# Kernel tuning notes

Hardware: AMD Instinct MI355X
Metric: run time of the kernel (lower is better)

## Reference

```python
import jax, jax.numpy as jnp
import numpy as np

LN_EPS = 1e-5
MODEL_DIM = 256
HEADS = 4


def layer_norm(x, gamma, beta):
    mu = jnp.mean(x, axis=-1, keepdims=True)
    var = jnp.var(x, axis=-1, keepdims=True)
    return (x - mu) * jax.lax.rsqrt(var + LN_EPS) * gamma + beta


def setup_inputs() -> dict:
    key = jax.random.key(0)
    ks = jax.random.split(key, 4)
    bs, s, d, h = 4, 2048, MODEL_DIM, HEADS
    x = jax.random.normal(ks[0], (bs, s, d), dtype=jnp.float32)
    Wq = jax.random.normal(ks[1], (d, h * d), dtype=jnp.float32) / np.sqrt(d)
    Wk = jax.random.normal(ks[2], (d, h * d), dtype=jnp.float32) / np.sqrt(d)
    Wv = jax.random.normal(ks[3], (h * d, d), dtype=jnp.float32) / np.sqrt(h * d)
    gamma = jnp.ones((d,), dtype=jnp.float32)
    beta = jnp.zeros((d,), dtype=jnp.float32)
    return {"x": x, "Wq": Wq, "Wk": Wk, "Wv": Wv, "gamma": gamma, "beta": beta}


def reference(x, Wq, Wk, Wv, gamma, beta):
    bs, s, d = x.shape
    h = Wq.shape[1] // d
    sqrt_norm = jnp.float32(np.sqrt(d))
    # pre_norm = False -> no input LN
    # NOTE: torch does .view(bs, h, s, d) on the (bs, s, h*d) projection --
    # a raw C-order reinterpretation, reproduced here by jnp.reshape.
    Q = jnp.reshape(x @ Wq, (bs, h, s, d))
    K = jnp.reshape(x @ Wk, (bs, h, s, d))
    scores = jnp.einsum('bhid,bhjd->bhij', Q, K)
    probs = jax.nn.softmax(scores / sqrt_norm, axis=-1)  # (bs, h, s, s)
    # value is the shared raw input x broadcast across heads
    out = jnp.einsum('bhij,bjd->bhid', probs, x)
    out = jnp.transpose(out, (0, 2, 1, 3)).reshape(bs, s, h * d)
    out = out @ Wv + x
    out = layer_norm(out, gamma, beta)  # post-norm
    return out, probs
```

## Files before the change

### kernel.cpp

```cpp
#include <hip/hip_runtime.h>

typedef __bf16 bf16;
typedef __bf16 bf16x8 __attribute__((ext_vector_type(8)));
typedef float f32x4 __attribute__((ext_vector_type(4)));

#define BS 4
#define S 2048
#define D 256
#define H 4
#define HD 1024
#define NROW 8192

__device__ __forceinline__ void load_lds16(const bf16* g, bf16* l) {
    __builtin_amdgcn_global_load_lds(
        (const __attribute__((address_space(1))) void*)g,
        (__attribute__((address_space(3))) void*)l, 16, 0, 0);
}

__global__ void prep_x(const float* __restrict__ x, bf16* __restrict__ x_bf,
                       bf16* __restrict__ xT_bf) {
    int idx = blockIdx.x * 256 + threadIdx.x;
    float v = x[idx];
    x_bf[idx] = (bf16)v;
    int dd = idx & (D - 1);
    int t = idx >> 8;
    int j = t & (S - 1);
    int b = t >> 11;
    xT_bf[(size_t)b * D * S + (size_t)dd * S + j] = (bf16)v;
}

__global__ void prep_w(const float* __restrict__ Wq, const float* __restrict__ Wk,
                       const float* __restrict__ Wv, bf16* __restrict__ WqT,
                       bf16* __restrict__ WkT, bf16* __restrict__ WvT) {
    int idx = blockIdx.x * 256 + threadIdx.x;
    const float SCALE = 0.09016844005556021f;
    int seg = idx >> 18;
    int r = idx & 262143;
    if (seg == 0) {
        int k = r & 255, n = r >> 8;
        WqT[r] = (bf16)(Wq[k * HD + n] * SCALE);
    } else if (seg == 1) {
        int k = r & 255, n = r >> 8;
        WkT[r] = (bf16)(Wk[k * HD + n]);
    } else {
        int k = r & 1023, n = r >> 10;
        WvT[r] = (bf16)(Wv[k * D + n]);
    }
}

__global__ __launch_bounds__(256) void gemm_nt_bf16(
    const bf16* __restrict__ A, const bf16* __restrict__ B0,
    const bf16* __restrict__ B1, bf16* __restrict__ C0, bf16* __restrict__ C1,
    int N, int Kd) {
    const bf16* B = blockIdx.z ? B1 : B0;
    bf16* C = blockIdx.z ? C1 : C0;
    int n0 = blockIdx.x * 64;
    int m0 = blockIdx.y * 64;
    __shared__ __align__(16) bf16 As[64 * 40];
    __shared__ __align__(16) bf16 Bs[64 * 40];
    int t = threadIdx.x, w = t >> 6, l = t & 63;
    int lr = l & 15, lq = l >> 4;
    f32x4 acc[4] = {};
    for (int k0 = 0; k0 < Kd; k0 += 32) {
        int row = t >> 2, cb = (t & 3) * 8;
        bf16x8 va = *(const bf16x8*)&A[(size_t)(m0 + row) * Kd + k0 + cb];
        *(bf16x8*)&As[row * 40 + cb] = va;
        bf16x8 vb = *(const bf16x8*)&B[(size_t)(n0 + row) * Kd + k0 + cb];
        *(bf16x8*)&Bs[row * 40 + cb] = vb;
        __syncthreads();
        bf16x8 af = *(const bf16x8*)&As[(w * 16 + lr) * 40 + lq * 8];
#pragma unroll
        for (int nt = 0; nt < 4; nt++) {
            bf16x8 bfr = *(const bf16x8*)&Bs[(nt * 16 + lr) * 40 + lq * 8];
            acc[nt] = __builtin_amdgcn_mfma_f32_16x16x32_bf16(af, bfr, acc[nt], 0, 0, 0);
        }
        __syncthreads();
    }
#pragma unroll
    for (int nt = 0; nt < 4; nt++)
#pragma unroll
        for (int rr = 0; rr < 4; rr++) {
            int row = m0 + w * 16 + lq * 4 + rr;
            C[(size_t)row * N + n0 + nt * 16 + lr] = (bf16)acc[nt][rr];
        }
}

__device__ __forceinline__ void stage_k_tile(const bf16* __restrict__ K,
                                             bf16* kb, int j0, int w, int l) {
    int krow = (w << 3) + (l >> 5);
    int kc = l & 31;
#pragma unroll
    for (int n = 0; n < 4; n++) {
        int r = krow + (n << 1);
        int cg = kc ^ ((r & 3) | ((r & 1) << 2));
        load_lds16(&K[(size_t)(j0 + r) * D + cg * 8], &kb[((w << 3) + (n << 1)) * 256]);
    }
}

__device__ __forceinline__ void stage_x_tile(const bf16* __restrict__ xTb,
                                             bf16* xb, int j0, int w, int l) {
    int xrow = (w << 6) + (l >> 2);
    int xc = l & 3;
#pragma unroll
    for (int n = 0; n < 4; n++) {
        int dd = xrow + (n << 4);
        int cg = xc ^ (dd & 3);
        load_lds16(&xTb[(size_t)dd * S + j0 + cg * 8], &xb[((w << 6) + (n << 4)) * 32]);
    }
}

__global__ __launch_bounds__(256, 2) void attn_fused(
    const bf16* __restrict__ Qbf, const bf16* __restrict__ Kbf,
    const bf16* __restrict__ xT, float* __restrict__ probs,
    bf16* __restrict__ attn) {
    int nblk = blockIdx.x;
    int lb = (nblk & 7) * 64 + (nblk >> 3);
    int bh = lb >> 5, b = bh >> 2, h = bh & 3;
    int t = threadIdx.x, w = t >> 6, l = t & 63;
    int lr = l & 15, lq = l >> 4;
    int sw = (lr & 3) | ((lr & 1) << 2);
    const bf16* Q = Qbf + (size_t)bh * S * D;
    const bf16* K = Kbf + (size_t)bh * S * D;
    const bf16* xTb = xT + (size_t)b * D * S;
    int ibase = (lb & 31) * 64 + w * 16;

    __shared__ __align__(16) bf16 kbuf[2][32 * 256];
    __shared__ __align__(16) bf16 xbuf[2][256 * 32];
    __shared__ __align__(16) bf16 pl[4][16 * 40];

    bf16x8 qf[8];
#pragma unroll
    for (int kf = 0; kf < 8; kf++)
        qf[kf] = *(const bf16x8*)&Q[(size_t)(ibase + lr) * D + kf * 32 + lq * 8];

    float lsum[4] = {0.f, 0.f, 0.f, 0.f};
    stage_k_tile(K, kbuf[0], 0, w, l);
    for (int it = 0; it < 64; it++) {
        int cur = it & 1;
        if (it < 63) {
            stage_k_tile(K, kbuf[cur ^ 1], (it + 1) << 5, w, l);
            asm volatile("s_waitcnt vmcnt(4)" ::: "memory");
        } else {
            asm volatile("s_waitcnt vmcnt(0)" ::: "memory");
        }
        __builtin_amdgcn_s_barrier();
#pragma unroll
        for (int subj = 0; subj < 2; subj++) {
            f32x4 acc = {};
#pragma unroll
            for (int kf = 0; kf < 8; kf++) {
                bf16x8 kfr = *(const bf16x8*)
                    &kbuf[cur][(subj * 16 + lr) * 256 + (((kf * 4 + lq) ^ sw) * 8)];
                acc = __builtin_amdgcn_mfma_f32_16x16x32_bf16(qf[kf], kfr, acc, 0, 0, 0);
            }
#pragma unroll
            for (int r = 0; r < 4; r++) lsum[r] += exp2f(acc[r]);
        }
        __builtin_amdgcn_s_barrier();
    }
    float li[4];
#pragma unroll
    for (int r = 0; r < 4; r++) {
        float s = lsum[r];
        for (int off = 1; off < 16; off <<= 1) s += __shfl_xor(s, off);
        li[r] = 1.0f / s;
    }

    f32x4 oacc[16] = {};
    float* probb = probs + (size_t)bh * S * S;
    stage_k_tile(K, kbuf[0], 0, w, l);
    stage_x_tile(xTb, xbuf[0], 0, w, l);
    for (int it = 0; it < 64; it++) {
        int cur = it & 1;
        int j0 = it << 5;
        if (it < 63) {
            stage_k_tile(K, kbuf[cur ^ 1], j0 + 32, w, l);
            stage_x_tile(xTb, xbuf[cur ^ 1], j0 + 32, w, l);
            asm volatile("s_waitcnt vmcnt(8)" ::: "memory");
        } else {
            asm volatile("s_waitcnt vmcnt(0)" ::: "memory");
        }
        __builtin_amdgcn_s_barrier();
#pragma unroll
        for (int subj = 0; subj < 2; subj++) {
            f32x4 acc = {};
#pragma unroll
            for (int kf = 0; kf < 8; kf++) {
                bf16x8 kfr = *(const bf16x8*)
                    &kbuf[cur][(subj * 16 + lr) * 256 + (((kf * 4 + lq) ^ sw) * 8)];
                acc = __builtin_amdgcn_mfma_f32_16x16x32_bf16(qf[kf], kfr, acc, 0, 0, 0);
            }
#pragma unroll
            for (int r = 0; r < 4; r++) {
                float p = exp2f(acc[r]) * li[r];
                pl[w][(lq * 4 + r) * 40 + subj * 16 + lr] = (bf16)p;
            }
        }
        bf16x8 pf = *(const bf16x8*)&pl[w][lr * 40 + lq * 8];
        f32x4 p0, p1;
#pragma unroll
        for (int e = 0; e < 4; e++) { p0[e] = (float)pf[e]; p1[e] = (float)pf[e + 4]; }
        float* pp = &probb[(size_t)(ibase + lr) * S + j0 + lq * 8];
        *(f32x4*)pp = p0;
        *(f32x4*)(pp + 4) = p1;
#pragma unroll
        for (int dt = 0; dt < 16; dt++) {
            int dd = dt * 16 + lr;
            bf16x8 xf = *(const bf16x8*)&xbuf[cur][dd * 32 + ((lq ^ (lr & 3)) * 8)];
            oacc[dt] = __builtin_amdgcn_mfma_f32_16x16x32_bf16(pf, xf, oacc[dt], 0, 0, 0);
        }
        __builtin_amdgcn_s_barrier();
    }
#pragma unroll
    for (int dt = 0; dt < 16; dt++)
#pragma unroll
        for (int rr = 0; rr < 4; rr++) {
            int row = ibase + lq * 4 + rr;
            attn[((size_t)(b * S + row)) * HD + h * D + dt * 16 + lr] = (bf16)oacc[dt][rr];
        }
}

__global__ __launch_bounds__(256) void out_gemm_ln(
    const bf16* __restrict__ attn, const bf16* __restrict__ WvT,
    const float* __restrict__ x, const float* __restrict__ gamma,
    const float* __restrict__ beta, float* __restrict__ out) {
    int m0 = blockIdx.x * 16;
    int t = threadIdx.x, w = t >> 6, l = t & 63;
    int lr = l & 15, lq = l >> 4;
    int ncol0 = w * 64;
    f32x4 acc[4] = {};
    for (int k0 = 0; k0 < HD; k0 += 32) {
        bf16x8 af = *(const bf16x8*)&attn[(size_t)(m0 + lr) * HD + k0 + lq * 8];
#pragma unroll
        for (int dt = 0; dt < 4; dt++) {
            bf16x8 bfr =
                *(const bf16x8*)&WvT[(size_t)(ncol0 + dt * 16 + lr) * HD + k0 + lq * 8];
            acc[dt] = __builtin_amdgcn_mfma_f32_16x16x32_bf16(af, bfr, acc[dt], 0, 0, 0);
        }
    }
    float sum[4] = {0, 0, 0, 0}, sq[4] = {0, 0, 0, 0};
#pragma unroll
    for (int dt = 0; dt < 4; dt++)
#pragma unroll
        for (int rr = 0; rr < 4; rr++) {
            int row = m0 + lq * 4 + rr;
            float v = acc[dt][rr] + x[(size_t)row * D + ncol0 + dt * 16 + lr];
            acc[dt][rr] = v;
            sum[rr] += v;
            sq[rr] += v * v;
        }
#pragma unroll
    for (int rr = 0; rr < 4; rr++)
        for (int off = 1; off < 16; off <<= 1) {
            sum[rr] += __shfl_xor(sum[rr], off);
            sq[rr] += __shfl_xor(sq[rr], off);
        }
    __shared__ float part[4][16][2];
    if (lr == 0)
#pragma unroll
        for (int rr = 0; rr < 4; rr++) {
            part[w][lq * 4 + rr][0] = sum[rr];
            part[w][lq * 4 + rr][1] = sq[rr];
        }
    __syncthreads();
    float mu[4], rs[4];
#pragma unroll
    for (int rr = 0; rr < 4; rr++) {
        int rowi = lq * 4 + rr;
        float s = part[0][rowi][0] + part[1][rowi][0] + part[2][rowi][0] + part[3][rowi][0];
        float q = part[0][rowi][1] + part[1][rowi][1] + part[2][rowi][1] + part[3][rowi][1];
        mu[rr] = s * (1.0f / 256.0f);
        float var = q * (1.0f / 256.0f) - mu[rr] * mu[rr];
        rs[rr] = rsqrtf(var + 1e-5f);
    }
#pragma unroll
    for (int dt = 0; dt < 4; dt++) {
        int col = ncol0 + dt * 16 + lr;
        float g = gamma[col], be = beta[col];
#pragma unroll
        for (int rr = 0; rr < 4; rr++) {
            float v = (acc[dt][rr] - mu[rr]) * rs[rr] * g + be;
            out[(size_t)(m0 + lq * 4 + rr) * D + col] = v;
        }
    }
}

extern "C" void kernel_launch(void* const* d_in, const int* in_sizes, int n_in,
                              void* d_out, int out_size, void* d_ws, size_t ws_size,
                              hipStream_t stream) {
    const float* x = (const float*)d_in[0];
    const float* Wq = (const float*)d_in[1];
    const float* Wk = (const float*)d_in[2];
    const float* Wv = (const float*)d_in[3];
    const float* gamma = (const float*)d_in[4];
    const float* beta = (const float*)d_in[5];
    float* out = (float*)d_out;
    float* probs = out + (size_t)NROW * D;

    char* ws = (char*)d_ws;
    bf16* x_bf = (bf16*)ws;
    bf16* xT_bf = (bf16*)(ws + 4194304);
    bf16* WqT = (bf16*)(ws + 8388608);
    bf16* WkT = (bf16*)(ws + 8912896);
    bf16* WvT = (bf16*)(ws + 9437184);
    bf16* Qbf = (bf16*)(ws + 9961472);
    bf16* Kbf = (bf16*)(ws + 26738688);
    bf16* attn = (bf16*)(ws + 43515904);

    prep_x<<<8192, 256, 0, stream>>>(x, x_bf, xT_bf);
    prep_w<<<3072, 256, 0, stream>>>(Wq, Wk, Wv, WqT, WkT, WvT);
    gemm_nt_bf16<<<dim3(16, 128, 2), 256, 0, stream>>>(x_bf, WqT, WkT, Qbf, Kbf,
                                                       HD, D);
    attn_fused<<<dim3(512), 256, 0, stream>>>(Qbf, Kbf, xT_bf, probs, attn);
    out_gemm_ln<<<512, 256, 0, stream>>>(attn, WvT, x, gamma, beta, out);
}
```

Measured before the change: 499.2 us.

## Tile transposes through LDS, stage full-K GEMM tiles, and retune LDS swizzles

After: 490.4 us. Within noise of the previous version (-1.8%).

```diff
diff --git a/kernel.cpp b/kernel.cpp
--- a/kernel.cpp
+++ b/kernel.cpp
@@ -1,6 +1,7 @@
 #include <hip/hip_runtime.h>
 
 typedef __bf16 bf16;
+typedef __bf16 bf16x4 __attribute__((ext_vector_type(4)));
 typedef __bf16 bf16x8 __attribute__((ext_vector_type(8)));
 typedef float f32x4 __attribute__((ext_vector_type(4)));
 
@@ -17,34 +18,86 @@
         (__attribute__((address_space(3))) void*)l, 16, 0, 0);
 }
 
-__global__ void prep_x(const float* __restrict__ x, bf16* __restrict__ x_bf,
-                       bf16* __restrict__ xT_bf) {
-    int idx = blockIdx.x * 256 + threadIdx.x;
-    float v = x[idx];
-    x_bf[idx] = (bf16)v;
-    int dd = idx & (D - 1);
-    int t = idx >> 8;
-    int j = t & (S - 1);
-    int b = t >> 11;
-    xT_bf[(size_t)b * D * S + (size_t)dd * S + j] = (bf16)v;
-}
-
-__global__ void prep_w(const float* __restrict__ Wq, const float* __restrict__ Wk,
-                       const float* __restrict__ Wv, bf16* __restrict__ WqT,
-                       bf16* __restrict__ WkT, bf16* __restrict__ WvT) {
-    int idx = blockIdx.x * 256 + threadIdx.x;
+__global__ __launch_bounds__(256) void prep_x(const float* __restrict__ x,
+                                              bf16* __restrict__ x_bf,
+                                              bf16* __restrict__ xT_bf) {
+    __shared__ bf16 tile[64][68];
+    int j0 = blockIdx.x * 64, d0 = blockIdx.y * 64, b = blockIdx.z;
+    int t = threadIdx.x;
+    int rsub = t >> 4;
+    int c4 = (t & 15) * 4;
+#pragma unroll
+    for (int rr = 0; rr < 4; rr++) {
+        int j = rr * 16 + rsub;
+        float4 v = *(const float4*)&x[((size_t)(b * S + j0 + j)) * D + d0 + c4];
+        bf16 b0 = (bf16)v.x, b1 = (bf16)v.y, b2 = (bf16)v.z, b3 = (bf16)v.w;
+        tile[j][c4 + 0] = b0;
+        tile[j][c4 + 1] = b1;
+        tile[j][c4 + 2] = b2;
+        tile[j][c4 + 3] = b3;
+        bf16x4 o = {b0, b1, b2, b3};
+        *(bf16x4*)&x_bf[((size_t)(b * S + j0 + j)) * D + d0 + c4] = o;
+    }
+    __syncthreads();
+#pragma unroll
+    for (int rr = 0; rr < 4; rr++) {
+        int dd = rr * 16 + rsub;
+        bf16x4 o;
+        o[0] = tile[c4 + 0][dd];
+        o[1] = tile[c4 + 1][dd];
+        o[2] = tile[c4 + 2][dd];
+        o[3] = tile[c4 + 3][dd];
+        *(bf16x4*)&xT_bf[(size_t)b * D * S + (size_t)(d0 + dd) * S + j0 + c4] = o;
+    }
+}
+
+__device__ __forceinline__ void tile_tr64(const float* __restrict__ src,
+                                          bf16* __restrict__ dst, int ldsrc,
+                                          int lddst, int r0, int c0, float scale,
+                                          bf16 (&tile)[64][68], int t) {
+    int rsub = t >> 4, c4 = (t & 15) * 4;
+#pragma unroll
+    for (int rr = 0; rr < 4; rr++) {
+        int r = rr * 16 + rsub;
+        float4 v = *(const float4*)&src[(size_t)(r0 + r) * ldsrc + c0 + c4];
+        tile[r][c4 + 0] = (bf16)(v.x * scale);
+        tile[r][c4 + 1] = (bf16)(v.y * scale);
+        tile[r][c4 + 2] = (bf16)(v.z * scale);
+        tile[r][c4 + 3] = (bf16)(v.w * scale);
+    }
+    __syncthreads();
+#pragma unroll
+    for (int rr = 0; rr < 4; rr++) {
+        int c = rr * 16 + rsub;
+        bf16x4 o;
+        o[0] = tile[c4 + 0][c];
+        o[1] = tile[c4 + 1][c];
+        o[2] = tile[c4 + 2][c];
+        o[3] = tile[c4 + 3][c];
+        *(bf16x4*)&dst[(size_t)(c0 + c) * lddst + r0 + c4] = o;
+    }
+}
+
+__global__ __launch_bounds__(256) void prep_w(const float* __restrict__ Wq,
+                                              const float* __restrict__ Wk,
+                                              const float* __restrict__ Wv,
+                                              bf16* __restrict__ WqT,
+                                              bf16* __restrict__ WkT,
+                                              bf16* __restrict__ WvT) {
+    __shared__ bf16 tile[64][68];
     const float SCALE = 0.09016844005556021f;
-    int seg = idx >> 18;
-    int r = idx & 262143;
-    if (seg == 0) {
-        int k = r & 255, n = r >> 8;
-        WqT[r] = (bf16)(Wq[k * HD + n] * SCALE);
-    } else if (seg == 1) {
-        int k = r & 255, n = r >> 8;
-        WkT[r] = (bf16)(Wk[k * HD + n]);
+    int bx = blockIdx.x, t = threadIdx.x;
+    if (bx < 64) {
+        int rt = bx & 3, ct = bx >> 2;
+        tile_tr64(Wq, WqT, HD, D, rt * 64, ct * 64, SCALE, tile, t);
+    } else if (bx < 128) {
+        int b2 = bx - 64;
+        int rt = b2 & 3, ct = b2 >> 2;
+        tile_tr64(Wk, WkT, HD, D, rt * 64, ct * 64, 1.0f, tile, t);
     } else {
-        int k = r & 1023, n = r >> 10;
-        WvT[r] = (bf16)(Wv[k * D + n]);
+        int b2 = bx - 128;
+        int rt = b2 & 15, ct = b2 >> 4;
+        tile_tr64(Wv, WvT, D, HD, rt * 64, ct * 64, 1.0f, tile, t);
     }
 }
 
@@ -56,25 +109,29 @@
     bf16* C = blockIdx.z ? C1 : C0;
     int n0 = blockIdx.x * 64;
     int m0 = blockIdx.y * 64;
-    __shared__ __align__(16) bf16 As[64 * 40];
-    __shared__ __align__(16) bf16 Bs[64 * 40];
+    __shared__ __align__(16) bf16 As[64 * 256];
+    __shared__ __align__(16) bf16 Bs[64 * 256];
     int t = threadIdx.x, w = t >> 6, l = t & 63;
     int lr = l & 15, lq = l >> 4;
+#pragma unroll
+    for (int n = 0; n < 8; n++) {
+        int r = w * 16 + 2 * n + (l >> 5);
+        int cg = (l & 31) ^ (r & 7);
+        load_lds16(&A[(size_t)(m0 + r) * D + cg * 8], &As[(w * 16 + 2 * n) * 256]);
+        load_lds16(&B[(size_t)(n0 + r) * D + cg * 8], &Bs[(w * 16 + 2 * n) * 256]);
+    }
+    asm volatile("s_waitcnt vmcnt(0)" ::: "memory");
+    __builtin_amdgcn_s_barrier();
     f32x4 acc[4] = {};
-    for (int k0 = 0; k0 < Kd; k0 += 32) {
-        int row = t >> 2, cb = (t & 3) * 8;
-        bf16x8 va = *(const bf16x8*)&A[(size_t)(m0 + row) * Kd + k0 + cb];
-        *(bf16x8*)&As[row * 40 + cb] = va;
-        bf16x8 vb = *(const bf16x8*)&B[(size_t)(n0 + row) * Kd + k0 + cb];
-        *(bf16x8*)&Bs[row * 40 + cb] = vb;
-        __syncthreads();
-        bf16x8 af = *(const bf16x8*)&As[(w * 16 + lr) * 40 + lq * 8];
+#pragma unroll
+    for (int kf = 0; kf < 8; kf++) {
+        bf16x8 af = *(const bf16x8*)&As[(w * 16 + lr) * 256 + (((kf * 4 + lq) ^ (lr & 7)) * 8)];
 #pragma unroll
         for (int nt = 0; nt < 4; nt++) {
-            bf16x8 bfr = *(const bf16x8*)&Bs[(nt * 16 + lr) * 40 + lq * 8];
+            bf16x8 bfr =
+                *(const bf16x8*)&Bs[(nt * 16 + lr) * 256 + (((kf * 4 + lq) ^ (lr & 7)) * 8)];
             acc[nt] = __builtin_amdgcn_mfma_f32_16x16x32_bf16(af, bfr, acc[nt], 0, 0, 0);
         }
-        __syncthreads();
     }
 #pragma unroll
     for (int nt = 0; nt < 4; nt++)
@@ -92,7 +149,7 @@
 #pragma unroll
     for (int n = 0; n < 4; n++) {
         int r = krow + (n << 1);
-        int cg = kc ^ ((r & 3) | ((r & 1) << 2));
+        int cg = kc ^ (r & 7);
         load_lds16(&K[(size_t)(j0 + r) * D + cg * 8], &kb[((w << 3) + (n << 1)) * 256]);
     }
 }
@@ -104,7 +161,7 @@
 #pragma unroll
     for (int n = 0; n < 4; n++) {
         int dd = xrow + (n << 4);
-        int cg = xc ^ (dd & 3);
+        int cg = xc ^ ((dd >> 1) & 3);
         load_lds16(&xTb[(size_t)dd * S + j0 + cg * 8], &xb[((w << 6) + (n << 4)) * 32]);
     }
 }
@@ -118,7 +175,6 @@
     int bh = lb >> 5, b = bh >> 2, h = bh & 3;
     int t = threadIdx.x, w = t >> 6, l = t & 63;
     int lr = l & 15, lq = l >> 4;
-    int sw = (lr & 3) | ((lr & 1) << 2);
     const bf16* Q = Qbf + (size_t)bh * S * D;
     const bf16* K = Kbf + (size_t)bh * S * D;
     const bf16* xTb = xT + (size_t)b * D * S;
@@ -150,7 +206,7 @@
 #pragma unroll
             for (int kf = 0; kf < 8; kf++) {
                 bf16x8 kfr = *(const bf16x8*)
-                    &kbuf[cur][(subj * 16 + lr) * 256 + (((kf * 4 + lq) ^ sw) * 8)];
+                    &kbuf[cur][(subj * 16 + lr) * 256 + (((kf * 4 + lq) ^ (lr & 7)) * 8)];
                 acc = __builtin_amdgcn_mfma_f32_16x16x32_bf16(qf[kf], kfr, acc, 0, 0, 0);
             }
 #pragma unroll
@@ -187,7 +243,7 @@
 #pragma unroll
             for (int kf = 0; kf < 8; kf++) {
                 bf16x8 kfr = *(const bf16x8*)
-                    &kbuf[cur][(subj * 16 + lr) * 256 + (((kf * 4 + lq) ^ sw) * 8)];
+                    &kbuf[cur][(subj * 16 + lr) * 256 + (((kf * 4 + lq) ^ (lr & 7)) * 8)];
                 acc = __builtin_amdgcn_mfma_f32_16x16x32_bf16(qf[kf], kfr, acc, 0, 0, 0);
             }
 #pragma unroll
@@ -206,7 +262,8 @@
 #pragma unroll
         for (int dt = 0; dt < 16; dt++) {
             int dd = dt * 16 + lr;
-            bf16x8 xf = *(const bf16x8*)&xbuf[cur][dd * 32 + ((lq ^ (lr & 3)) * 8)];
+            bf16x8 xf =
+                *(const bf16x8*)&xbuf[cur][dd * 32 + ((lq ^ ((lr >> 1) & 3)) * 8)];
             oacc[dt] = __builtin_amdgcn_mfma_f32_16x16x32_bf16(pf, xf, oacc[dt], 0, 0, 0);
         }
         __builtin_amdgcn_s_barrier();
@@ -307,8 +364,8 @@
     bf16* Kbf = (bf16*)(ws + 26738688);
     bf16* attn = (bf16*)(ws + 43515904);
 
-    prep_x<<<8192, 256, 0, stream>>>(x, x_bf, xT_bf);
-    prep_w<<<3072, 256, 0, stream>>>(Wq, Wk, Wv, WqT, WkT, WvT);
+    prep_x<<<dim3(32, 4, 4), 256, 0, stream>>>(x, x_bf, xT_bf);
+    prep_w<<<192, 256, 0, stream>>>(Wq, Wk, Wv, WqT, WkT, WvT);
     gemm_nt_bf16<<<dim3(16, 128, 2), 256, 0, stream>>>(x_bf, WqT, WkT, Qbf, Kbf,
                                                        HD, D);
     attn_fused<<<dim3(512), 256, 0, stream>>>(Qbf, Kbf, xT_bf, probs, attn);
```
